# Performance work log

Hardware: AMD Instinct MI355X
Metric: run time of the kernel (lower is better)

## Reference

```python
import jax, jax.numpy as jnp
import numpy as np

# ---- static config (matches init_kwargs cfg) ----
N_IMGS, C_FEAT = 9, 24
HF, WF = 112, 112            # quarter-res feature map
H_IMG, W_IMG = 448, 448      # CDR.IMG_SIZE
HD, WD = 56, 56              # DEPTH_PRED_SIZE
N_PLANES = 64                # DEPTH_MVS.N_INTERVALS
DEPTH_START, DEPTH_INTERVAL = 0.5, 0.05
EDGES_PER_REF = 8
N_EDGES = N_IMGS * EDGES_PER_REF
N_PIX = HD * WD


def setup_inputs() -> dict:
    key = jax.random.key(0)
    k1, k2, k3, k4 = jax.random.split(key, 4)
    feats_quarter = jax.random.normal(k1, (N_IMGS, C_FEAT, HF, WF), jnp.float32)
    # proper rotation matrices via QR so the camera math is well conditioned
    A = jax.random.normal(k2, (N_IMGS, 3, 3), jnp.float32)
    rotmats, _ = jnp.linalg.qr(A)
    rotmats = rotmats.astype(jnp.float32)
    tvecs = 0.1 * jax.random.normal(k3, (N_IMGS, 3), jnp.float32)
    K = jnp.broadcast_to(
        jnp.array([[400.0, 0.0, (W_IMG - 1) / 2.0],
                   [0.0, 400.0, (H_IMG - 1) / 2.0],
                   [0.0, 0.0, 1.0]], jnp.float32), (N_IMGS, 3, 3))
    # ref index sorted+repeated so unique(return_inverse) == ref row itself
    ref = jnp.repeat(jnp.arange(N_IMGS, dtype=jnp.int32), EDGES_PER_REF)
    src = jax.random.randint(k4, (N_EDGES,), 0, N_IMGS, dtype=jnp.int32)
    ref_src_edges = jnp.stack([ref, src], 0)
    return {"feats_quarter": feats_quarter, "rotmats": rotmats,
            "tvecs": tvecs, "K": K, "ref_src_edges": ref_src_edges}


def _forward(feats_quarter, rotmats, tvecs, K, ref_src_edges):
    ref_e, src_e = ref_src_edges[0], ref_src_edges[1]

    # ---- batched_build_plane_sweep_volume_tensor: world-space points per ref view ----
    us = jnp.linspace(0.0, W_IMG - 1.0, WD)
    vs = jnp.linspace(0.0, H_IMG - 1.0, HD)
    uu, vv = jnp.meshgrid(us, vs)                              # [HD, WD]
    pix = jnp.stack([uu, vv, jnp.ones_like(uu)], 0).reshape(3, N_PIX)
    rays = jnp.einsum('nij,jp->nip', jnp.linalg.inv(K), pix)  # [N, 3, P]
    depths = DEPTH_START + DEPTH_INTERVAL * jnp.arange(N_PLANES, dtype=jnp.float32)
    pts_cam = rays[:, None] * depths[None, :, None, None]      # [N, D, 3, P] (plane-major)
    pts_cam = pts_cam.transpose(0, 2, 1, 3).reshape(N_IMGS, 3, N_PLANES * N_PIX)
    pts_world = jnp.einsum('nji,njp->nip', rotmats, pts_cam - tvecs[:, :, None])
    n_pts = N_PLANES * N_PIX

    # ---- project ref-volume points into each src view (per edge) ----
    pts_homo = jnp.concatenate([pts_world, jnp.ones((N_IMGS, 1, n_pts), jnp.float32)], 1)
    P = jnp.einsum('nij,njk->nik', K, jnp.concatenate([rotmats, tvecs[:, :, None]], 2))  # [N,3,4]
    proj = jnp.einsum('eij,ejp->eip', P[src_e], pts_homo[ref_e])  # [E, 3, n_pts]
    z = jnp.abs(proj[:, 2]) + 1e-8
    gx = proj[:, 0] / z / (W_IMG - 1.0) * 2.0 - 1.0
    gy = proj[:, 1] / z / (H_IMG - 1.0) * 2.0 - 1.0

    # ---- bilinear grid_sample, align_corners=True, zeros padding ----
    def sample_one(img, gx1, gy1):  # img [C,HF,WF], gx1/gy1 [n_pts]
        x = (gx1 + 1.0) * 0.5 * (WF - 1)
        y = (gy1 + 1.0) * 0.5 * (HF - 1)
        x0 = jnp.floor(x)
        y0 = jnp.floor(y)
        wx1 = x - x0
        wy1 = y - y0

        def tap(xi, yi, w):
            valid = (xi >= 0) & (xi <= WF - 1) & (yi >= 0) & (yi <= HF - 1)
            xc = jnp.clip(xi, 0, WF - 1).astype(jnp.int32)
            yc = jnp.clip(yi, 0, HF - 1).astype(jnp.int32)
            return jnp.where(valid, w, 0.0)[None] * img[:, yc, xc]  # [C, n_pts]

        return (tap(x0, y0, (1 - wx1) * (1 - wy1))
                + tap(x0 + 1, y0, wx1 * (1 - wy1))
                + tap(x0, y0 + 1, (1 - wx1) * wy1)
                + tap(x0 + 1, y0 + 1, wx1 * wy1))

    x_vox = jax.vmap(sample_one)(feats_quarter[src_e], gx, gy)   # [E, C, n_pts]
    x_vox = x_vox.reshape(N_EDGES, C_FEAT, N_PLANES, HD, WD)

    # ---- scatter mean / sq-mean over edges sharing a ref image, then variance ----
    counts = jax.ops.segment_sum(jnp.ones((N_EDGES,), jnp.float32), ref_e, num_segments=N_IMGS)
    denom = jnp.maximum(counts, 1.0)[:, None, None, None, None]
    x_avg = jax.ops.segment_sum(x_vox, ref_e, num_segments=N_IMGS) / denom
    x_avg_sq = jax.ops.segment_sum(x_vox ** 2, ref_e, num_segments=N_IMGS) / denom
    return x_avg_sq - x_avg ** 2  # [n_ref, C, D, HD, WD]


def reference(feats_quarter, rotmats, tvecs, K, ref_src_edges):
    return _forward(feats_quarter, rotmats, tvecs, K, ref_src_edges)
```

## Files before the change

### kernel.cpp

```cpp
#include <hip/hip_runtime.h>

constexpr int kNImgs   = 9;
constexpr int kC       = 24;
constexpr int kHF      = 112, kWF = 112;
constexpr int kHD      = 56,  kWD = 56;
constexpr int kNPix    = kHD * kWD;
constexpr int kNPlanes = 64;
constexpr int kPtsPerRef = kNPlanes * kNPix;
constexpr int kEdgesPerRef = 8;
constexpr int kNEdges  = kNImgs * kEdgesPerRef;
constexpr int kFeatPix = kHF * kWF;
constexpr int kFeatPerImg = kC * kFeatPix;

constexpr int kDTile = 32, kPTile = 32;
constexpr int kDHalves = kNPlanes / kDTile;
constexpr int kPGroups = kNPix / kPTile;
constexpr int kBlocksPerRef = kDHalves * kPGroups;

typedef _Float16 half8 __attribute__((ext_vector_type(8)));

__device__ inline void mm3(const float* A, const float* B, float* C) {
#pragma unroll
  for (int i = 0; i < 3; ++i)
#pragma unroll
    for (int j = 0; j < 3; ++j)
      C[i*3+j] = A[i*3+0]*B[0*3+j] + A[i*3+1]*B[1*3+j] + A[i*3+2]*B[2*3+j];
}

__device__ inline void inv3(const float* A, float* I) {
  float a=A[0],b=A[1],c=A[2],d=A[3],e=A[4],f=A[5],g=A[6],h=A[7],i=A[8];
  float c00 = e*i - f*h;
  float c01 = -(d*i - f*g);
  float c02 = d*h - e*g;
  float det = a*c00 + b*c01 + c*c02;
  float r = 1.0f / det;
  I[0] = c00*r;           I[1] = (c*h - b*i)*r;  I[2] = (b*f - c*e)*r;
  I[3] = c01*r;           I[4] = (a*i - c*g)*r;  I[5] = (c*d - a*f)*r;
  I[6] = c02*r;           I[7] = (b*g - a*h)*r;  I[8] = (a*e - b*d)*r;
}

__global__ __launch_bounds__(256)
void transpose_feats_kernel(const float* __restrict__ f, _Float16* __restrict__ ft) {
  int idx = blockIdx.x * 256 + threadIdx.x;
  if (idx >= kNImgs * kFeatPerImg) return;
  int n  = idx / kFeatPerImg;
  int r  = idx - n * kFeatPerImg;
  int c  = r / kFeatPix;
  int yx = r - c * kFeatPix;
  ft[((size_t)n * kFeatPix + yx) * kC + c] = (_Float16)f[idx];
}

template <bool TR>
__global__ __launch_bounds__(1024, 4)
void psv_var_kernel(const float* __restrict__ feats,
                    const _Float16* __restrict__ featsT,
                    const float* __restrict__ rotmats,
                    const float* __restrict__ tvecs,
                    const float* __restrict__ Kmat,
                    const int*   __restrict__ edges,
                    float* __restrict__ out) {
  __shared__ float sM[kEdgesPerRef][9];
  __shared__ float sB[kEdgesPerRef][3];
  __shared__ int   sSrc[kEdgesPerRef];
  __shared__ int   sUIdx[kEdgesPerRef];
  __shared__ float sMult[kEdgesPerRef];
  __shared__ int   sKU;
  __shared__ float sT[4][kDTile][kPTile + 1];

  const int nwg = gridDim.x;
  const int orig = blockIdx.x;
  const int q = nwg >> 3, r8 = nwg & 7;
  const int xcd = orig & 7, lin = orig >> 3;
  const int bid = ((xcd < r8) ? xcd * (q + 1) : r8 * (q + 1) + (xcd - r8) * q) + lin;

  const int n     = bid / kBlocksPerRef;
  const int rem   = bid - n * kBlocksPerRef;
  const int dHalf = rem / kPGroups;
  const int pG    = rem - dHalf * kPGroups;

  const int t = threadIdx.x;

  if (t < kEdgesPerRef) {
    const int e  = n * kEdgesPerRef + t;
    const int re = edges[e];
    const int se = edges[kNEdges + e];
    sSrc[t] = se;

    const float* Rr = rotmats + re * 9;
    const float* Rs = rotmats + se * 9;
    const float* Kr = Kmat + re * 9;
    const float* Ks = Kmat + se * 9;
    const float* tr = tvecs + re * 3;
    const float* ts = tvecs + se * 3;

    float RrT[9];
#pragma unroll
    for (int i = 0; i < 3; ++i)
#pragma unroll
      for (int j = 0; j < 3; ++j) RrT[i*3+j] = Rr[j*3+i];

    float Kinv[9], A[9], T1[9], M[9];
    inv3(Kr, Kinv);
    mm3(Rs, RrT, A);
    mm3(A, Kinv, T1);
    mm3(Ks, T1, M);

    float At0 = A[0]*tr[0] + A[1]*tr[1] + A[2]*tr[2];
    float At1 = A[3]*tr[0] + A[4]*tr[1] + A[5]*tr[2];
    float At2 = A[6]*tr[0] + A[7]*tr[1] + A[8]*tr[2];
    float bv0 = ts[0] - At0, bv1 = ts[1] - At1, bv2 = ts[2] - At2;
#pragma unroll
    for (int i = 0; i < 9; ++i) sM[t][i] = M[i];
#pragma unroll
    for (int i = 0; i < 3; ++i)
      sB[t][i] = Ks[i*3+0]*bv0 + Ks[i*3+1]*bv1 + Ks[i*3+2]*bv2;
  }
  __syncthreads();

  if (t == 0) {
    int k = 0;
    for (int j = 0; j < kEdgesPerRef; ++j) {
      const int s = sSrc[j];
      bool dup = false;
      for (int i = 0; i < k; ++i) {
        if (sSrc[sUIdx[i]] == s) { sMult[i] += 1.0f; dup = true; break; }
      }
      if (!dup) { sUIdx[k] = j; sMult[k] = 1.0f; ++k; }
    }
    sKU = k;
  }
  __syncthreads();

  const int dsub = t & 31;
  const int psub = t >> 5;
  const int d = dHalf * kDTile + dsub;
  const int p = pG * kPTile + psub;
  const int h = p / kWD;
  const int w = p - h * kWD;

  const float u = (float)w * (447.0f / 55.0f);
  const float v = (float)h * (447.0f / 55.0f);
  const float depth = 0.5f + 0.05f * (float)d;

  float acc[kC], accsq[kC];
#pragma unroll
  for (int c = 0; c < kC; ++c) { acc[c] = 0.0f; accsq[c] = 0.0f; }

  const int kU = sKU;
#pragma unroll 2
  for (int jj = 0; jj < kU; ++jj) {
    const int j = sUIdx[jj];
    const float mult = sMult[jj];
    const float* M = sM[j];
    const float px = depth * (M[0]*u + M[1]*v + M[2]) + sB[j][0];
    const float py = depth * (M[3]*u + M[4]*v + M[5]) + sB[j][1];
    const float pz = depth * (M[6]*u + M[7]*v + M[8]) + sB[j][2];
    const float rz = 1.0f / (fabsf(pz) + 1e-8f);

    const float x = px * rz * (111.0f / 447.0f);
    const float y = py * rz * (111.0f / 447.0f);

    const float x0 = floorf(x), y0 = floorf(y);
    const float wx = x - x0, wy = y - y0;
    const bool vx0 = (x0 >= 0.0f)  && (x0 <= 111.0f);
    const bool vx1 = (x0 >= -1.0f) && (x0 <= 110.0f);
    const bool vy0 = (y0 >= 0.0f)  && (y0 <= 111.0f);
    const bool vy1 = (y0 >= -1.0f) && (y0 <= 110.0f);
    const float w00 = (vx0 && vy0) ? (1.0f - wx) * (1.0f - wy) : 0.0f;
    const float w01 = (vx1 && vy0) ? wx * (1.0f - wy) : 0.0f;
    const float w10 = (vx0 && vy1) ? (1.0f - wx) * wy : 0.0f;
    const float w11 = (vx1 && vy1) ? wx * wy : 0.0f;

    const int xc0 = (int)fminf(fmaxf(x0,        0.0f), 111.0f);
    const int xc1 = (int)fminf(fmaxf(x0 + 1.0f, 0.0f), 111.0f);
    const int yc0 = (int)fminf(fmaxf(y0,        0.0f), 111.0f);
    const int yc1 = (int)fminf(fmaxf(y0 + 1.0f, 0.0f), 111.0f);

    const int src = sSrc[j];
    if constexpr (TR) {
      const _Float16* base = featsT + (size_t)src * kFeatPix * kC;
      const int o00 = (yc0 * kWF + xc0) * kC;
      const int o01 = (yc0 * kWF + xc1) * kC;
      const int o10 = (yc1 * kWF + xc0) * kC;
      const int o11 = (yc1 * kWF + xc1) * kC;
#pragma unroll
      for (int i = 0; i < kC / 8; ++i) {
        const half8 f00 = *(const half8*)(base + o00 + 8*i);
        const half8 f01 = *(const half8*)(base + o01 + 8*i);
        const half8 f10 = *(const half8*)(base + o10 + 8*i);
        const half8 f11 = *(const half8*)(base + o11 + 8*i);
#pragma unroll
        for (int k = 0; k < 8; ++k) {
          float val = w00 * (float)f00[k] + w01 * (float)f01[k]
                    + w10 * (float)f10[k] + w11 * (float)f11[k];
          const int c = 8*i + k;
          const float mval = mult * val;
          acc[c] += mval;
          accsq[c] = __builtin_fmaf(mval, val, accsq[c]);
        }
      }
    } else {
      const float* base = feats + (size_t)src * kFeatPerImg;
      const int o00 = yc0 * kWF + xc0;
      const int o01 = yc0 * kWF + xc1;
      const int o10 = yc1 * kWF + xc0;
      const int o11 = yc1 * kWF + xc1;
#pragma unroll
      for (int c = 0; c < kC; ++c) {
        const float* bc = base + c * kFeatPix;
        float val = w00*bc[o00] + w01*bc[o01] + w10*bc[o10] + w11*bc[o11];
        const float mval = mult * val;
        acc[c] += mval;
        accsq[c] = __builtin_fmaf(mval, val, accsq[c]);
      }
    }
  }

  const int pp2 = t & 31;
  const int dd2 = t >> 5;
  const size_t outBase = (size_t)n * kC * (size_t)kPtsPerRef;
#pragma unroll
  for (int ch = 0; ch < kC / 4; ++ch) {
    __syncthreads();
#pragma unroll
    for (int cc = 0; cc < 4; ++cc) {
      const int c = ch * 4 + cc;
      const float mean = acc[c] * 0.125f;
      const float msq  = accsq[c] * 0.125f;
      sT[cc][dsub][psub] = msq - mean * mean;
    }
    __syncthreads();
#pragma unroll
    for (int cc = 0; cc < 4; ++cc) {
      const int c = ch * 4 + cc;
      out[outBase + ((size_t)c * kNPlanes + (dHalf * kDTile + dd2)) * kNPix
          + pG * kPTile + pp2] = sT[cc][dd2][pp2];
    }
  }
}

extern "C" void kernel_launch(void* const* d_in, const int* in_sizes, int n_in,
                              void* d_out, int out_size, void* d_ws, size_t ws_size,
                              hipStream_t stream) {
  const float* feats  = (const float*)d_in[0];
  const float* rot    = (const float*)d_in[1];
  const float* tv     = (const float*)d_in[2];
  const float* Kmat   = (const float*)d_in[3];
  const int*   edges  = (const int*)d_in[4];
  float* out = (float*)d_out;

  const size_t featsTBytes = (size_t)kNImgs * kFeatPix * kC * sizeof(_Float16);
  const int gridMain = kNImgs * kBlocksPerRef;

  if (ws_size >= featsTBytes) {
    _Float16* featsT = (_Float16*)d_ws;
    const int nT = kNImgs * kFeatPerImg;
    transpose_feats_kernel<<<(nT + 255) / 256, 256, 0, stream>>>(feats, featsT);
    psv_var_kernel<true><<<gridMain, 1024, 0, stream>>>(feats, featsT, rot, tv, Kmat, edges, out);
  } else {
    psv_var_kernel<false><<<gridMain, 1024, 0, stream>>>(feats, nullptr, rot, tv, Kmat, edges, out);
  }
}
```

Baseline: 171.2 us.

## Use packed fp16 bilinear interpolation and smaller 256-thread tiles

Performs the four-tap bilinear blend in packed half2 arithmetic on raw 32-bit loads, converting to float only for the accumulation into float2 mean and square-mean registers. Shrinks the pixel tile from 32 to 8 so blocks are 256 threads, and restructures the shared-memory transpose for the output write into two phases of 12 channels. The aim is to halve the VALU work of the interpolation and improve scheduling and occupancy. In exchange, interpolated values lose precision because of fp16 arithmetic, and the output stores are now 8 contiguous floats per row instead of 32.

```diff
diff --git a/kernel.cpp b/kernel.cpp
--- a/kernel.cpp
+++ b/kernel.cpp
@@ -12,12 +12,19 @@
 constexpr int kFeatPix = kHF * kWF;
 constexpr int kFeatPerImg = kC * kFeatPix;
 
-constexpr int kDTile = 32, kPTile = 32;
+constexpr int kDTile = 32, kPTile = 8;
 constexpr int kDHalves = kNPlanes / kDTile;
 constexpr int kPGroups = kNPix / kPTile;
 constexpr int kBlocksPerRef = kDHalves * kPGroups;
 
-typedef _Float16 half8 __attribute__((ext_vector_type(8)));
+typedef _Float16 half8  __attribute__((ext_vector_type(8)));
+typedef _Float16 half2v __attribute__((ext_vector_type(2)));
+typedef float    float2v __attribute__((ext_vector_type(2)));
+typedef unsigned int uint4v __attribute__((ext_vector_type(4)));
+
+__device__ inline half2v u2h(unsigned int u) {
+  union { unsigned int u; half2v h; } cv; cv.u = u; return cv.h;
+}
 
 __device__ inline void mm3(const float* A, const float* B, float* C) {
 #pragma unroll
@@ -51,7 +58,7 @@
 }
 
 template <bool TR>
-__global__ __launch_bounds__(1024, 4)
+__global__ __launch_bounds__(256)
 void psv_var_kernel(const float* __restrict__ feats,
                     const _Float16* __restrict__ featsT,
                     const float* __restrict__ rotmats,
@@ -65,7 +72,7 @@
   __shared__ int   sUIdx[kEdgesPerRef];
   __shared__ float sMult[kEdgesPerRef];
   __shared__ int   sKU;
-  __shared__ float sT[4][kDTile][kPTile + 1];
+  __shared__ float sT[kC / 2][kPTile][kDTile + 2];
 
   const int nwg = gridDim.x;
   const int orig = blockIdx.x;
@@ -142,12 +149,15 @@
   const float v = (float)h * (447.0f / 55.0f);
   const float depth = 0.5f + 0.05f * (float)d;
 
-  float acc[kC], accsq[kC];
-#pragma unroll
-  for (int c = 0; c < kC; ++c) { acc[c] = 0.0f; accsq[c] = 0.0f; }
+  float2v acc2[kC / 2], accsq2[kC / 2];
+#pragma unroll
+  for (int i = 0; i < kC / 2; ++i) {
+    acc2[i] = (float2v){0.0f, 0.0f};
+    accsq2[i] = (float2v){0.0f, 0.0f};
+  }
 
   const int kU = sKU;
-#pragma unroll 2
+
   for (int jj = 0; jj < kU; ++jj) {
     const int j = sUIdx[jj];
     const float mult = sMult[jj];
@@ -178,6 +188,11 @@
 
     const int src = sSrc[j];
     if constexpr (TR) {
+      const _Float16 h00 = (_Float16)w00, h01 = (_Float16)w01;
+      const _Float16 h10 = (_Float16)w10, h11 = (_Float16)w11;
+      const half2v w00p = {h00, h00}, w01p = {h01, h01};
+      const half2v w10p = {h10, h10}, w11p = {h11, h11};
+      const float2v mult2 = {mult, mult};
       const _Float16* base = featsT + (size_t)src * kFeatPix * kC;
       const int o00 = (yc0 * kWF + xc0) * kC;
       const int o01 = (yc0 * kWF + xc1) * kC;
@@ -185,18 +200,19 @@
       const int o11 = (yc1 * kWF + xc1) * kC;
 #pragma unroll
       for (int i = 0; i < kC / 8; ++i) {
-        const half8 f00 = *(const half8*)(base + o00 + 8*i);
-        const half8 f01 = *(const half8*)(base + o01 + 8*i);
-        const half8 f10 = *(const half8*)(base + o10 + 8*i);
-        const half8 f11 = *(const half8*)(base + o11 + 8*i);
-#pragma unroll
-        for (int k = 0; k < 8; ++k) {
-          float val = w00 * (float)f00[k] + w01 * (float)f01[k]
-                    + w10 * (float)f10[k] + w11 * (float)f11[k];
-          const int c = 8*i + k;
-          const float mval = mult * val;
-          acc[c] += mval;
-          accsq[c] = __builtin_fmaf(mval, val, accsq[c]);
+        const uint4v q00 = *(const uint4v*)(base + o00 + 8*i);
+        const uint4v q01 = *(const uint4v*)(base + o01 + 8*i);
+        const uint4v q10 = *(const uint4v*)(base + o10 + 8*i);
+        const uint4v q11 = *(const uint4v*)(base + o11 + 8*i);
+#pragma unroll
+        for (int k2 = 0; k2 < 4; ++k2) {
+          const half2v val2h = u2h(q00[k2]) * w00p + u2h(q01[k2]) * w01p
+                             + u2h(q10[k2]) * w10p + u2h(q11[k2]) * w11p;
+          const float2v val2 = {(float)val2h[0], (float)val2h[1]};
+          const float2v mval2 = mult2 * val2;
+          const int idx = i*4 + k2;
+          acc2[idx] += mval2;
+          accsq2[idx] = mval2 * val2 + accsq2[idx];
         }
       }
     } else {
@@ -206,35 +222,40 @@
       const int o10 = yc1 * kWF + xc0;
       const int o11 = yc1 * kWF + xc1;
 #pragma unroll
-      for (int c = 0; c < kC; ++c) {
-        const float* bc = base + c * kFeatPix;
-        float val = w00*bc[o00] + w01*bc[o01] + w10*bc[o10] + w11*bc[o11];
-        const float mval = mult * val;
-        acc[c] += mval;
-        accsq[c] = __builtin_fmaf(mval, val, accsq[c]);
+      for (int i = 0; i < kC / 2; ++i) {
+#pragma unroll
+        for (int kk = 0; kk < 2; ++kk) {
+          const int c = 2*i + kk;
+          const float* bc = base + (size_t)c * kFeatPix;
+          float val = w00*bc[o00] + w01*bc[o01] + w10*bc[o10] + w11*bc[o11];
+          const float mval = mult * val;
+          acc2[i][kk] += mval;
+          accsq2[i][kk] = __builtin_fmaf(mval, val, accsq2[i][kk]);
+        }
       }
     }
   }
 
-  const int pp2 = t & 31;
-  const int dd2 = t >> 5;
+  const int pp2 = t & (kPTile - 1);
+  const int dd2 = t >> 3;
   const size_t outBase = (size_t)n * kC * (size_t)kPtsPerRef;
 #pragma unroll
-  for (int ch = 0; ch < kC / 4; ++ch) {
+  for (int ph = 0; ph < 2; ++ph) {
     __syncthreads();
 #pragma unroll
-    for (int cc = 0; cc < 4; ++cc) {
-      const int c = ch * 4 + cc;
-      const float mean = acc[c] * 0.125f;
-      const float msq  = accsq[c] * 0.125f;
-      sT[cc][dsub][psub] = msq - mean * mean;
+    for (int cc = 0; cc < kC / 2; ++cc) {
+      const int c = ph * (kC / 2) + cc;
+      const float a = acc2[c >> 1][c & 1];
+      const float s = accsq2[c >> 1][c & 1];
+      const float mean = a * 0.125f;
+      sT[cc][psub][dsub] = s * 0.125f - mean * mean;
     }
     __syncthreads();
 #pragma unroll
-    for (int cc = 0; cc < 4; ++cc) {
-      const int c = ch * 4 + cc;
+    for (int cc = 0; cc < kC / 2; ++cc) {
+      const int c = ph * (kC / 2) + cc;
       out[outBase + ((size_t)c * kNPlanes + (dHalf * kDTile + dd2)) * kNPix
-          + pG * kPTile + pp2] = sT[cc][dd2][pp2];
+          + pG * kPTile + pp2] = sT[cc][pp2][dd2];
     }
   }
 }
@@ -256,8 +277,8 @@
     _Float16* featsT = (_Float16*)d_ws;
     const int nT = kNImgs * kFeatPerImg;
     transpose_feats_kernel<<<(nT + 255) / 256, 256, 0, stream>>>(feats, featsT);
-    psv_var_kernel<true><<<gridMain, 1024, 0, stream>>>(feats, featsT, rot, tv, Kmat, edges, out);
+    psv_var_kernel<true><<<gridMain, 256, 0, stream>>>(feats, featsT, rot, tv, Kmat, edges, out);
   } else {
-    psv_var_kernel<false><<<gridMain, 1024, 0, stream>>>(feats, nullptr, rot, tv, Kmat, edges, out);
-  }
-}
+    psv_var_kernel<false><<<gridMain, 256, 0, stream>>>(feats, nullptr, rot, tv, Kmat, edges, out);
+  }
+}
```

Result: faster. 151.6 us (-11.4%).
